# Kernel optimization log

Hardware: AMD Instinct MI355X
Metric: run time of the kernel (lower is better)

## Reference

```python
import jax, jax.numpy as jnp
import numpy as np

B, S, E, P, H, F = 4, 4096, 256, 32, 8, 1024
DH = E // H
LN_EPS = 1e-5


def setup_inputs() -> dict:
    key = jax.random.key(0)
    ks = jax.random.split(key, 12)
    dt = jnp.float32
    return {
        "src": jax.random.normal(ks[0], (B, S, E), dt),
        "pos_embed": jax.random.normal(ks[1], (B, P, S), dt),
        # learnable positional transform (pos_linear: P -> P)
        "Wpos": jax.random.normal(ks[2], (P, P), dt) * (1.0 / np.sqrt(P)),
        "bpos": jnp.zeros((P,), dt),
        # RBF kernel hyperparameters (ScaleKernel(RBFKernel)) -- positive scalars
        "lengthscale": jnp.full((), 2.0, dt),
        "outputscale": jnp.full((), 1.0, dt),
        # value / output projections of multihead attention
        "Wv": jax.random.normal(ks[3], (E, E), dt) * (1.0 / np.sqrt(E)),
        "bv": jnp.zeros((E,), dt),
        "Wo": jax.random.normal(ks[4], (E, E), dt) * (1.0 / np.sqrt(E)),
        "bo": jnp.zeros((E,), dt),
        # feed-forward
        "W1": jax.random.normal(ks[5], (F, E), dt) * (1.0 / np.sqrt(E)),
        "b1": jnp.zeros((F,), dt),
        "W2": jax.random.normal(ks[6], (E, F), dt) * (1.0 / np.sqrt(F)),
        "b2": jnp.zeros((E,), dt),
        # layer norms
        "ln1_g": jnp.ones((E,), dt), "ln1_b": jnp.zeros((E,), dt),
        "ln2_g": jnp.ones((E,), dt), "ln2_b": jnp.zeros((E,), dt),
    }


def _layer_norm(x, g, b):
    mu = jnp.mean(x, -1, keepdims=True)
    var = jnp.mean(jnp.square(x - mu), -1, keepdims=True)
    return (x - mu) * jax.lax.rsqrt(var + LN_EPS) * g + b


def _rbf_scores(x, lengthscale, outputscale):
    # x: [B, S, P] -> scaled RBF kernel matrix [B, S, S]
    xs = x / lengthscale
    sq = jnp.sum(xs * xs, axis=-1)  # [B, S]
    d2 = sq[:, :, None] + sq[:, None, :] - 2.0 * jnp.einsum('bsp,btp->bst', xs, xs)
    d2 = jnp.maximum(d2, 0.0)
    return outputscale * jnp.exp(-0.5 * d2)


def reference(src, pos_embed, Wpos, bpos, lengthscale, outputscale,
              Wv, bv, Wo, bo, W1, b1, W2, b2, ln1_g, ln1_b, ln2_g, ln2_b):
    b, s, e = src.shape
    # learnable positional transform: [B,P,S] -> [B,S,P] -> linear -> back
    pe = jnp.einsum('bps,op->bos', pos_embed, Wpos) + bpos[None, :, None]  # [B,P,S]
    # GP-kernel attention scores over sequence positions
    scores = _rbf_scores(pe.transpose(0, 2, 1), lengthscale, outputscale)  # [B,S,S]
    attn = jax.nn.softmax(scores, axis=-1)
    # value projection, per-head weighted sum (scores shared across heads)
    v = (src @ Wv.T + bv).reshape(b, s, H, DH)
    ctx = jnp.einsum('bqk,bkhd->bqhd', attn, v).reshape(b, s, e)
    attn_out = ctx @ Wo.T + bo
    x = _layer_norm(src + attn_out, ln1_g, ln1_b)
    ff = jax.nn.relu(x @ W1.T + b1) @ W2.T + b2
    return _layer_norm(x + ff, ln2_g, ln2_b)
```

## Files before the change

kernel.cpp:

```cpp
#include <hip/hip_runtime.h>
#include <stdint.h>

#define BN 4
#define SN 4096
#define EN 256
#define PN 32
#define FN 1024
#define BS (BN*SN)
#define PAUG 64

typedef uint16_t bf16_t;
typedef short v4s  __attribute__((ext_vector_type(4)));
typedef short v8s  __attribute__((ext_vector_type(8)));
typedef __bf16 bf16x8 __attribute__((ext_vector_type(8)));
typedef float v4f   __attribute__((ext_vector_type(4)));
typedef float v16f  __attribute__((ext_vector_type(16)));

#define MFMA16(a,b,c) __builtin_amdgcn_mfma_f32_16x16x32_bf16(a,b,c,0,0,0)
#define MFMA32(a,b,c) __builtin_amdgcn_mfma_f32_32x32x16_bf16(a,b,c,0,0,0)

__device__ __forceinline__ float b2f(bf16_t x){
    uint32_t u = ((uint32_t)x) << 16; float f; __builtin_memcpy(&f, &u, 4); return f;
}
__device__ __forceinline__ bf16_t f2b(float f){
    uint32_t u; __builtin_memcpy(&u, &f, 4);
    u += 0x7FFFu + ((u >> 16) & 1u);
    return (bf16_t)(u >> 16);
}
__device__ __forceinline__ bf16x8 ldb8(const bf16_t* p){
    v8s r = *(const v8s*)p; return __builtin_bit_cast(bf16x8, r);
}
__device__ __forceinline__ bf16x8 ldb8u(const bf16_t* p){
    v4s lo = *(const v4s*)p;
    v4s hi = *(const v4s*)(p + 4);
    v8s r = __builtin_shufflevector(lo, hi, 0,1,2,3,4,5,6,7);
    return __builtin_bit_cast(bf16x8, r);
}
__device__ __forceinline__ float ldsc(const float* p){ return *p; }
__device__ __forceinline__ float ldsc(const bf16_t* p){ return b2f(*p); }
__device__ __forceinline__ void stsc(float* p, float v){ *p = v; }
__device__ __forceinline__ void stsc(bf16_t* p, float v){ *p = f2b(v); }

#if __has_builtin(__builtin_amdgcn_exp2f)
__device__ __forceinline__ float fexp2(float x){ return __builtin_amdgcn_exp2f(x); }
#else
__device__ __forceinline__ float fexp2(float x){ return exp2f(x); }
#endif

#if __has_builtin(__builtin_amdgcn_cvt_pk_bf16_f32)
typedef __bf16 bf16x2 __attribute__((ext_vector_type(2)));
__device__ __forceinline__ uint32_t pkbf16(float a, float b){
    bf16x2 r = __builtin_amdgcn_cvt_pk_bf16_f32(a, b);
    return __builtin_bit_cast(uint32_t, r);
}
#else
__device__ __forceinline__ uint32_t pkbf16(float a, float b){
    return (uint32_t)f2b(a) | ((uint32_t)f2b(b) << 16);
}
#endif

typedef const __attribute__((address_space(1))) uint32_t* glds_gp;
typedef __attribute__((address_space(3))) uint32_t* glds_lp;
__device__ __forceinline__ void glds16(const bf16_t* g, bf16_t* l){
    __builtin_amdgcn_global_load_lds((glds_gp)g, (glds_lp)l, 16, 0, 0);
}

__global__ __launch_bounds__(256) void prep_kernel(
    const float* __restrict__ src, bf16_t* __restrict__ srcb,
    const float* __restrict__ Wv, bf16_t* __restrict__ Wvb,
    const float* __restrict__ Wo, bf16_t* __restrict__ Wob,
    const float* __restrict__ W1, bf16_t* __restrict__ W1b,
    const float* __restrict__ W2, bf16_t* __restrict__ W2b,
    const float* __restrict__ pos, const float* __restrict__ Wp,
    const float* __restrict__ bp,  const float* __restrict__ lsp,
    bf16_t* __restrict__ xk, bf16_t* __restrict__ xq)
{
    __shared__ float Wsh[PN*PN];
    __shared__ float bsh[PN];
    int bid = blockIdx.x;
    int tid = threadIdx.x;

    if (bid < 4736){
        const float* sp; bf16_t* dp; int off;
        if (bid < 4096){ sp = src; dp = srcb; off = (bid*256 + tid)*4; }
        else {
            int i = ((bid - 4096)*256 + tid)*4;
            if      (i <  65536){ sp=Wv; dp=Wvb; off=i; }
            else if (i < 131072){ sp=Wo; dp=Wob; off=i- 65536; }
            else if (i < 393216){ sp=W1; dp=W1b; off=i-131072; }
            else                { sp=W2; dp=W2b; off=i-393216; }
        }
        float4 f = *(const float4*)(sp + off);
        v4s o;
        o.x = (short)f2b(f.x); o.y = (short)f2b(f.y);
        o.z = (short)f2b(f.z); o.w = (short)f2b(f.w);
        *(v4s*)(dp + off) = o;
        return;
    }

    int pb = bid - 4736;
    int b  = pb >> 4;
    int s  = (pb & 15)*256 + tid;

    for (int i = tid; i < PN*PN; i += 256) Wsh[i] = Wp[i];
    if (tid < PN) bsh[tid] = bp[tid];
    __syncthreads();

    float inv_ls = 1.0f / lsp[0];
    const float c1f = 1.4426950408889634f;

    float col[PN];
    #pragma unroll
    for (int p = 0; p < PN; p++) col[p] = pos[((size_t)b*PN + p)*SN + s];

    uint16_t xb[PN], qb[PN];
    float sq = 0.f;
    #pragma unroll 4
    for (int o = 0; o < PN; o++){
        float pe = bsh[o];
        #pragma unroll
        for (int p = 0; p < PN; p++) pe += col[p] * Wsh[o*PN + p];
        float pv = pe * inv_ls;
        uint16_t h = f2b(pv);
        xb[o] = h;
        qb[o] = f2b(c1f * pv);
        float xr = b2f(h);
        sq += xr * xr;
    }

    size_t base = ((size_t)b*SN + s) * PAUG;
    v8s pk[8];
    #pragma unroll
    for (int c = 0; c < 4; c++)
        #pragma unroll
        for (int j = 0; j < 8; j++) ((short*)&pk[c])[j] = (short)xb[c*8 + j];
    #pragma unroll
    for (int c = 4; c < 8; c++)
        #pragma unroll
        for (int j = 0; j < 8; j++) ((short*)&pk[c])[j] = 0;
    ((short*)&pk[4])[0] = (short)f2b(-0.5f * sq);
    ((short*)&pk[4])[1] = (short)0x3F80;
    #pragma unroll
    for (int c = 0; c < 8; c++) *(v8s*)(xk + base + c*8) = pk[c];

    #pragma unroll
    for (int c = 0; c < 4; c++)
        #pragma unroll
        for (int j = 0; j < 8; j++) ((short*)&pk[c])[j] = (short)qb[c*8 + j];
    ((short*)&pk[4])[0] = (short)f2b(c1f);
    ((short*)&pk[4])[1] = (short)f2b(-0.5f * sq * c1f);
    #pragma unroll
    for (int c = 0; c < 8; c++) *(v8s*)(xq + base + c*8) = pk[c];
}

template<int EPI, typename OutT>
__global__ __launch_bounds__(256) void gemm_t(
    const bf16_t* __restrict__ A, const bf16_t* __restrict__ W,
    const float* __restrict__ bias, OutT* __restrict__ out,
    bf16_t* __restrict__ vt, int N, int K)
{
    __shared__ __align__(16) bf16_t At[2][4096];
    __shared__ __align__(16) bf16_t Wt[2][4096];
    int tid = threadIdx.x;
    int lane = tid & 63, wv = tid >> 6, col = lane & 15, quad = lane >> 4;
    int m0 = blockIdx.x * 64, n0 = blockIdx.y * 64;
    int nck = K >> 6;

    int srow = tid >> 3;
    int spc  = (tid & 7) ^ (srow & 7);
    const bf16_t* asrc = A + (size_t)(m0 + srow)*K + spc*8;
    const bf16_t* wsrc = W + (size_t)(n0 + srow)*K + spc*8;

    v4f acc[4];
    #pragma unroll
    for (int t = 0; t < 4; t++) acc[t] = (v4f){0.f,0.f,0.f,0.f};

    glds16(asrc, &At[0][tid*8]);
    glds16(asrc + (size_t)32*K, &At[0][2048 + tid*8]);
    glds16(wsrc, &Wt[0][tid*8]);
    glds16(wsrc + (size_t)32*K, &Wt[0][2048 + tid*8]);
    __syncthreads();

    for (int c = 0; c < nck; c++){
        int cb = c & 1;
        if (c + 1 < nck){
            glds16(asrc + (c+1)*64, &At[cb^1][tid*8]);
            glds16(asrc + (size_t)32*K + (c+1)*64, &At[cb^1][2048 + tid*8]);
            glds16(wsrc + (c+1)*64, &Wt[cb^1][tid*8]);
            glds16(wsrc + (size_t)32*K + (c+1)*64, &Wt[cb^1][2048 + tid*8]);
        }
        #pragma unroll
        for (int kc = 0; kc < 2; kc++){
            int pc = ((kc*4 + quad) ^ (col & 7)) * 8;
            bf16x8 a = ldb8(&At[cb][(wv*16 + col)*64 + pc]);
            #pragma unroll
            for (int t = 0; t < 4; t++){
                bf16x8 b = ldb8(&Wt[cb][(t*16 + col)*64 + pc]);
                acc[t] = MFMA16(a, b, acc[t]);
            }
        }
        __syncthreads();
    }

    float bfv[4];
    #pragma unroll
    for (int t = 0; t < 4; t++) bfv[t] = bias[n0 + t*16 + col];

    if constexpr (EPI == 3){
        __shared__ uint16_t Tsh[64*74];
        #pragma unroll
        for (int r = 0; r < 4; r++)
            #pragma unroll
            for (int t = 0; t < 4; t++)
                Tsh[(wv*16 + quad*4 + r)*74 + t*16 + col] = f2b(acc[t][r] + bfv[t]);
        __syncthreads();
        int e = tid >> 2, sc = tid & 3;
        int b = m0 >> 12;
        int sbat = m0 & (SN-1);
        int eb   = (n0 + e) >> 5;
        int l31e = (n0 + e) & 31;
        int k16  = (sbat >> 4) + sc;
        v8s p0, p1;
        #pragma unroll
        for (int i = 0; i < 8; i++) ((short*)&p0)[i] = (short)Tsh[(sc*16 + i)*74 + e];
        #pragma unroll
        for (int i = 0; i < 8; i++) ((short*)&p1)[i] = (short)Tsh[(sc*16 + 8 + i)*74 + e];
        bf16_t* dst = vt + ((((size_t)b*8 + eb)*256 + k16)*64 + l31e)*8;
        *(v8s*)dst = p0;
        *(v8s*)(dst + 256) = p1;
    } else {
        #pragma unroll
        for (int r = 0; r < 4; r++){
            int row = m0 + wv*16 + quad*4 + r;
            #pragma unroll
            for (int t = 0; t < 4; t++){
                float y = acc[t][r] + bfv[t];
                if constexpr (EPI == 1) y = fmaxf(y, 0.f);
                stsc(out + (size_t)row*N + n0 + t*16 + col, y);
            }
        }
    }
}

template<int EPI>
__global__ __launch_bounds__(256, 2) void gemm128(
    const bf16_t* __restrict__ A, const bf16_t* __restrict__ W,
    const float* __restrict__ bias, bf16_t* __restrict__ out,
    int N, int K)
{
    __shared__ __align__(16) bf16_t At[2][8192];
    __shared__ __align__(16) bf16_t Wt[2][8192];
    int tid = threadIdx.x;
    int lane = tid & 63, wv = tid >> 6, col = lane & 15, quad = lane >> 4;
    int m0 = blockIdx.x * 128, n0 = blockIdx.y * 128;
    int nck = K >> 6;

    int srow = tid >> 3;
    int spc  = (tid & 7) ^ (srow & 7);
    const bf16_t* asrc = A + (size_t)(m0 + srow)*K + spc*8;
    const bf16_t* wsrc = W + (size_t)(n0 + srow)*K + spc*8;

    v4f acc[2][8];
    #pragma unroll
    for (int mi = 0; mi < 2; mi++)
        #pragma unroll
        for (int t = 0; t < 8; t++) acc[mi][t] = (v4f){0.f,0.f,0.f,0.f};

    #pragma unroll
    for (int s = 0; s < 4; s++){
        glds16(asrc + (size_t)(s*32)*K, &At[0][s*2048 + tid*8]);
        glds16(wsrc + (size_t)(s*32)*K, &Wt[0][s*2048 + tid*8]);
    }
    __syncthreads();

    for (int c = 0; c < nck; c++){
        int cb = c & 1;
        if (c + 1 < nck){
            #pragma unroll
            for (int s = 0; s < 4; s++){
                glds16(asrc + (size_t)(s*32)*K + (c+1)*64, &At[cb^1][s*2048 + tid*8]);
                glds16(wsrc + (size_t)(s*32)*K + (c+1)*64, &Wt[cb^1][s*2048 + tid*8]);
            }
        }
        #pragma unroll
        for (int kc = 0; kc < 2; kc++){
            int pc = ((kc*4 + quad) ^ (col & 7)) * 8;
            bf16x8 a[2];
            #pragma unroll
            for (int mi = 0; mi < 2; mi++)
                a[mi] = ldb8(&At[cb][(wv*32 + mi*16 + col)*64 + pc]);
            #pragma unroll
            for (int t = 0; t < 8; t++){
                bf16x8 b = ldb8(&Wt[cb][(t*16 + col)*64 + pc]);
                #pragma unroll
                for (int mi = 0; mi < 2; mi++)
                    acc[mi][t] = MFMA16(a[mi], b, acc[mi][t]);
            }
        }
        __syncthreads();
    }

    float bfv[8];
    #pragma unroll
    for (int t = 0; t < 8; t++) bfv[t] = bias[n0 + t*16 + col];

    #pragma unroll
    for (int mi = 0; mi < 2; mi++){
        #pragma unroll
        for (int r = 0; r < 4; r++){
            int row = m0 + wv*32 + mi*16 + quad*4 + r;
            #pragma unroll
            for (int t = 0; t < 8; t++){
                float y = acc[mi][t][r] + bfv[t];
                if constexpr (EPI == 1) y = fmaxf(y, 0.f);
                out[(size_t)row*N + n0 + t*16 + col] = f2b(y);
            }
        }
    }
}

template<typename OutT>
__global__ __launch_bounds__(512, 4) void gemm_ln(
    const bf16_t* __restrict__ A, const bf16_t* __restrict__ W,
    const float* __restrict__ bias, const bf16_t* __restrict__ res,
    const float* __restrict__ gamma, const float* __restrict__ beta,
    OutT* __restrict__ out, int K)
{
    __shared__ __align__(16) bf16_t At[2][32*64];
    __shared__ __align__(16) bf16_t Wt[2][256*64];
    __shared__ float lnb[4][32][2];

    int tid = threadIdx.x;
    int lane = tid & 63, wv = tid >> 6, col = lane & 15, quad = lane >> 4;
    int mw = wv >> 2;
    int nw = wv & 3;
    int m0 = blockIdx.x * 32;
    int nck = K >> 6;

    int arow = (tid & 255) >> 3;
    int apc  = (tid & 7) ^ (arow & 7);
    const bf16_t* asrc = A + (size_t)(m0 + arow)*K + apc*8;
    int wr0  = tid >> 3;
    const bf16_t* wsrc[4];
    #pragma unroll
    for (int s = 0; s < 4; s++){
        int wrow = s*64 + wr0;
        int wpc  = (tid & 7) ^ (wrow & 7);
        wsrc[s] = W + (size_t)wrow*K + wpc*8;
    }

    v4f acc[4];
    #pragma unroll
    for (int t = 0; t < 4; t++) acc[t] = (v4f){0.f,0.f,0.f,0.f};

    if (tid < 256) glds16(asrc, &At[0][tid*8]);
    #pragma unroll
    for (int s = 0; s < 4; s++) glds16(wsrc[s], &Wt[0][s*4096 + tid*8]);
    __syncthreads();

    for (int c = 0; c < nck; c++){
        int cb = c & 1;
        if (c + 1 < nck){
            if (tid < 256) glds16(asrc + (c+1)*64, &At[cb^1][tid*8]);
            #pragma unroll
            for (int s = 0; s < 4; s++)
                glds16(wsrc[s] + (c+1)*64, &Wt[cb^1][s*4096 + tid*8]);
        }
        #pragma unroll
        for (int kc = 0; kc < 2; kc++){
            int pc = ((kc*4 + quad) ^ (col & 7)) * 8;
            bf16x8 a = ldb8(&At[cb][(mw*16 + col)*64 + pc]);
            #pragma unroll
            for (int t = 0; t < 4; t++){
                bf16x8 b = ldb8(&Wt[cb][(nw*64 + t*16 + col)*64 + pc]);
                acc[t] = MFMA16(a, b, acc[t]);
            }
        }
        __syncthreads();
    }

    float bfv[4];
    #pragma unroll
    for (int t = 0; t < 4; t++) bfv[t] = bias[nw*64 + t*16 + col];

    float v[4][4];
    float s1[4], s2[4];
    #pragma unroll
    for (int r = 0; r < 4; r++){ s1[r] = 0.f; s2[r] = 0.f; }
    #pragma unroll
    for (int r = 0; r < 4; r++){
        int row = m0 + mw*16 + quad*4 + r;
        #pragma unroll
        for (int t = 0; t < 4; t++){
            float x = acc[t][r] + bfv[t]
                    + b2f(res[(size_t)row*EN + nw*64 + t*16 + col]);
            v[t][r] = x; s1[r] += x; s2[r] += x*x;
        }
    }
    #pragma unroll
    for (int r = 0; r < 4; r++){
        #pragma unroll
        for (int m = 1; m <= 8; m <<= 1){
            s1[r] += __shfl_xor(s1[r], m);
            s2[r] += __shfl_xor(s2[r], m);
        }
    }
    if (col == 0){
        #pragma unroll
        for (int r = 0; r < 4; r++){
            int rl = mw*16 + quad*4 + r;
            lnb[nw][rl][0] = s1[r];
            lnb[nw][rl][1] = s2[r];
        }
    }
    __syncthreads();
    #pragma unroll
    for (int r = 0; r < 4; r++){
        int rl  = mw*16 + quad*4 + r;
        int row = m0 + rl;
        float S1 = lnb[0][rl][0] + lnb[1][rl][0] + lnb[2][rl][0] + lnb[3][rl][0];
        float S2 = lnb[0][rl][1] + lnb[1][rl][1] + lnb[2][rl][1] + lnb[3][rl][1];
        float mu = S1 * (1.f/256.f);
        float rs = rsqrtf(S2 * (1.f/256.f) - mu*mu + 1e-5f);
        #pragma unroll
        for (int t = 0; t < 4; t++){
            int gi = nw*64 + t*16 + col;
            stsc(out + (size_t)row*EN + gi, (v[t][r]-mu)*rs*gamma[gi] + beta[gi]);
        }
    }
}

__global__ __launch_bounds__(512, 4) void attn_kernel(
    const bf16_t* __restrict__ xk, const bf16_t* __restrict__ xq,
    const bf16_t* __restrict__ vf, const float* __restrict__ osp,
    bf16_t* __restrict__ ctx)
{
    __shared__ __align__(16) bf16_t Wtb[2][64*132];
    __shared__ __align__(16) bf16_t Qs[64*64];
    __shared__ float densh[8][64];
    __shared__ float dent[64];

    int tid  = threadIdx.x;
    int lane = tid & 63;
    int wv   = tid >> 6;
    int col  = lane & 15;
    int quad = lane >> 4;
    int l31  = lane & 31;
    int half = lane >> 5;

    int bid = blockIdx.x;
    int b   = (bid & 7) >> 1;
    int qi  = ((bid >> 3) << 1) | (bid & 1);
    int q0  = qi * 64;

    float k2 = 1.4426950408889634f * osp[0];

    const bf16_t* xkb = xk + (size_t)b * SN * PAUG;
    const bf16_t* xqb = xq + (size_t)b * SN * PAUG;
    const bf16_t* vfb = vf + (((size_t)b*8 + wv)*256)*512 + lane*8;

    {
        int qrow = tid >> 3;
        int qpc  = (tid & 7) ^ (qrow & 7);
        glds16(xqb + (size_t)(q0 + qrow)*PAUG + qpc*8, &Qs[tid*8]);
    }

    v16f acc[2];
    #pragma unroll
    for (int qg = 0; qg < 2; qg++)
        #pragma unroll
        for (int i = 0; i < 16; i++) acc[qg][i] = 0.f;
    float den[4] = {0.f, 0.f, 0.f, 0.f};
    const v4f zero = (v4f){0.f,0.f,0.f,0.f};

    bf16x8 kf0, kf1;
    {
        const bf16_t* kr = xkb + (size_t)(wv*16 + col)*PAUG + quad*8;
        kf0 = ldb8(kr); kf1 = ldb8(kr + 32);
    }

    __syncthreads();

    for (int c = 0; c < 32; c++){
        int cb = c & 1;
        bf16x8 vr[8];
        #pragma unroll
        for (int sk = 0; sk < 8; sk++)
            vr[sk] = ldb8(vfb + (size_t)(c*8 + sk)*512);

        #pragma unroll
        for (int qg = 0; qg < 2; qg++){
            #pragma unroll
            for (int g2 = 0; g2 < 2; g2++){
                int qr = qg*32 + g2*16 + col;
                bf16x8 qa = ldb8(&Qs[qr*64 + ((quad    ) ^ (col & 7))*8]);
                bf16x8 qb = ldb8(&Qs[qr*64 + ((4 + quad) ^ (col & 7))*8]);
                v4f st = MFMA16(kf0, qa, zero);
                st = MFMA16(kf1, qb, st);
                #pragma unroll
                for (int rp = 0; rp < 2; rp++){
                    float w0 = fexp2(fmaf(k2, fexp2(st[rp*2+0]), -k2));
                    float w1 = fexp2(fmaf(k2, fexp2(st[rp*2+1]), -k2));
                    den[qg*2+g2] += w0 + w1;
                    *(uint32_t*)&Wtb[cb][qr*132 + wv*16 + quad*4 + rp*2]
                        = pkbf16(w0, w1);
                }
            }
        }

        if (c + 1 < 32){
            const bf16_t* kr = xkb + (size_t)((c+1)*128 + wv*16 + col)*PAUG + quad*8;
            kf0 = ldb8(kr); kf1 = ldb8(kr + 32);
        }

        asm volatile("s_waitcnt lgkmcnt(0)" ::: "memory");
        __builtin_amdgcn_s_barrier();
        __builtin_amdgcn_sched_barrier(0);

        #pragma unroll
        for (int qg = 0; qg < 2; qg++){
            #pragma unroll
            for (int sk4 = 0; sk4 < 2; sk4++){
                bf16x8 af[4];
                #pragma unroll
                for (int j = 0; j < 4; j++)
                    af[j] = ldb8u(&Wtb[cb][(qg*32 + l31)*132 + (sk4*4 + j)*16 + half*8]);
                #pragma unroll
                for (int j = 0; j < 4; j++)
                    acc[qg] = MFMA32(af[j], vr[sk4*4 + j], acc[qg]);
            }
        }
    }

    #pragma unroll
    for (int d = 0; d < 4; d++){
        den[d] += __shfl_xor(den[d], 16);
        den[d] += __shfl_xor(den[d], 32);
    }
    if (lane < 16){
        #pragma unroll
        for (int qg = 0; qg < 2; qg++)
            #pragma unroll
            for (int g2 = 0; g2 < 2; g2++)
                densh[wv][qg*32 + g2*16 + lane] = den[qg*2+g2];
    }
    __syncthreads();
    if (tid < 64){
        float s = 0.f;
        #pragma unroll
        for (int w = 0; w < 8; w++) s += densh[w][tid];
        dent[tid] = 1.f / s;
    }
    __syncthreads();

    size_t obase = ((size_t)b*SN + q0) * EN + wv*32;
    #pragma unroll
    for (int qg = 0; qg < 2; qg++){
        #pragma unroll
        for (int rg = 0; rg < 16; rg++){
            int row = (rg & 3) + 8*(rg >> 2) + 4*half;
            float inv = dent[qg*32 + row];
            ctx[obase + (size_t)(qg*32 + row)*EN + l31] = f2b(acc[qg][rg] * inv);
        }
    }
}

extern "C" void kernel_launch(void* const* d_in, const int* in_sizes, int n_in,
                              void* d_out, int out_size, void* d_ws, size_t ws_size,
                              hipStream_t stream)
{
    (void)in_sizes; (void)n_in; (void)out_size; (void)ws_size;
    const float* src  = (const float*)d_in[0];
    const float* pos  = (const float*)d_in[1];
    const float* Wpos = (const float*)d_in[2];
    const float* bpos = (const float*)d_in[3];
    const float* ls   = (const float*)d_in[4];
    const float* os   = (const float*)d_in[5];
    const float* Wv   = (const float*)d_in[6];
    const float* bv   = (const float*)d_in[7];
    const float* Wo   = (const float*)d_in[8];
    const float* bo   = (const float*)d_in[9];
    const float* W1   = (const float*)d_in[10];
    const float* b1   = (const float*)d_in[11];
    const float* W2   = (const float*)d_in[12];
    const float* b2   = (const float*)d_in[13];
    const float* g1   = (const float*)d_in[14];
    const float* be1  = (const float*)d_in[15];
    const float* g2   = (const float*)d_in[16];
    const float* be2  = (const float*)d_in[17];

    char* w = (char*)d_ws;
    bf16_t* xkb  = (bf16_t*)(w);
    bf16_t* xqb  = (bf16_t*)(w + ( 2u<<20));
    bf16_t* Wvb  = (bf16_t*)(w + ( 4u<<20));
    bf16_t* Wob  = (bf16_t*)(w + ( 4u<<20) + (1u<<18));
    bf16_t* W1b  = (bf16_t*)(w + ( 5u<<20));
    bf16_t* W2b  = (bf16_t*)(w + ( 6u<<20));
    bf16_t* srcb = (bf16_t*)(w + ( 8u<<20));
    bf16_t* vtg  = (bf16_t*)(w + (16u<<20));
    bf16_t* ctx  = (bf16_t*)(w + (24u<<20));
    bf16_t* xws  = (bf16_t*)(w + (24u<<20));
    bf16_t* hws  = (bf16_t*)(w + (32u<<20));

    prep_kernel<<<dim3(4800), 256, 0, stream>>>(
        src, srcb, Wv, Wvb, Wo, Wob, W1, W1b, W2, W2b,
        pos, Wpos, bpos, ls, xkb, xqb);

    gemm_t<3, bf16_t><<<dim3(BS/64, EN/64), 256, 0, stream>>>(
        srcb, Wvb, bv, (bf16_t*)nullptr, vtg, EN, EN);
    attn_kernel<<<dim3(256), 512, 0, stream>>>(xkb, xqb, vtg, os, ctx);
    gemm_ln<bf16_t><<<dim3(BS/32), 512, 0, stream>>>(
        ctx, Wob, bo, srcb, g1, be1, xws, EN);
    gemm128<1><<<dim3(BS/128, FN/128), 256, 0, stream>>>(
        xws, W1b, b1, hws, FN, EN);
    gemm_ln<float><<<dim3(BS/32), 512, 0, stream>>>(
        hws, W2b, b2, xws, g2, be2, (float*)d_out, FN);
}
```

Baseline: 232.5 us.

## Fuse output projection, residual and LayerNorm into attention kernel epilogue

The attention kernel now writes its normalized context tile into shared memory and runs the Wo projection with MFMA, then adds bias and residual and applies LayerNorm 1 before writing x. This removes the ctx round trip through global memory and one kernel launch. Wo is pre-swizzled into an MFMA-fragment layout in the prep kernel, and launch bounds drop from 4 to 2 blocks per CU. The extra 32KB of shared memory and added registers may reduce occupancy of the attention phase.

```diff
diff --git a/kernel.cpp b/kernel.cpp
--- a/kernel.cpp
+++ b/kernel.cpp
@@ -86,7 +86,17 @@
         else {
             int i = ((bid - 4096)*256 + tid)*4;
             if      (i <  65536){ sp=Wv; dp=Wvb; off=i; }
-            else if (i < 131072){ sp=Wo; dp=Wob; off=i- 65536; }
+            else if (i < 131072){
+                int idx = i - 65536;
+                float4 f = *(const float4*)(Wo + idx);
+                v4s o;
+                o.x = (short)f2b(f.x); o.y = (short)f2b(f.y);
+                o.z = (short)f2b(f.z); o.w = (short)f2b(f.w);
+                int n = idx >> 8, k = idx & 255;
+                int dst = (((n>>4)*8 + (k>>5))*64 + (((k>>3)&3)*16 + (n&15)))*8 + (k&7);
+                *(v4s*)(Wob + dst) = o;
+                return;
+            }
             else if (i < 393216){ sp=W1; dp=W1b; off=i-131072; }
             else                { sp=W2; dp=W2b; off=i-393216; }
         }
@@ -430,15 +440,19 @@
     }
 }
 
-__global__ __launch_bounds__(512, 4) void attn_kernel(
+__global__ __launch_bounds__(512, 2) void attn_kernel(
     const bf16_t* __restrict__ xk, const bf16_t* __restrict__ xq,
     const bf16_t* __restrict__ vf, const float* __restrict__ osp,
-    bf16_t* __restrict__ ctx)
+    const bf16_t* __restrict__ wof, const float* __restrict__ bo,
+    const bf16_t* __restrict__ res, const float* __restrict__ gamma,
+    const float* __restrict__ beta, bf16_t* __restrict__ out)
 {
     __shared__ __align__(16) bf16_t Wtb[2][64*132];
     __shared__ __align__(16) bf16_t Qs[64*64];
+    __shared__ __align__(16) bf16_t Osh[64*256];
     __shared__ float densh[8][64];
     __shared__ float dent[64];
+    __shared__ float lnw[8][64][2];
 
     int tid  = threadIdx.x;
     int lane = tid & 63;
@@ -553,14 +567,74 @@
     }
     __syncthreads();
 
-    size_t obase = ((size_t)b*SN + q0) * EN + wv*32;
     #pragma unroll
     for (int qg = 0; qg < 2; qg++){
         #pragma unroll
         for (int rg = 0; rg < 16; rg++){
-            int row = (rg & 3) + 8*(rg >> 2) + 4*half;
-            float inv = dent[qg*32 + row];
-            ctx[obase + (size_t)(qg*32 + row)*EN + l31] = f2b(acc[qg][rg] * inv);
+            int qrow = qg*32 + (rg & 3) + 8*(rg >> 2) + 4*half;
+            int e = wv*32 + l31;
+            int g = e >> 3;
+            Osh[qrow*256 + ((g ^ (qrow & 7))*8) + (e & 7)] = f2b(acc[qg][rg] * dent[qrow]);
+        }
+    }
+    __syncthreads();
+
+    v4f y[4][2];
+    #pragma unroll
+    for (int qg = 0; qg < 4; qg++)
+        #pragma unroll
+        for (int t = 0; t < 2; t++) y[qg][t] = (v4f){0.f,0.f,0.f,0.f};
+
+    #pragma unroll
+    for (int kc = 0; kc < 8; kc++){
+        bf16x8 b0 = ldb8(wof + (size_t)(((wv*2+0)*8 + kc)*64 + lane)*8);
+        bf16x8 b1 = ldb8(wof + (size_t)(((wv*2+1)*8 + kc)*64 + lane)*8);
+        #pragma unroll
+        for (int qg = 0; qg < 4; qg++){
+            bf16x8 a = ldb8(&Osh[(qg*16 + col)*256 + (((kc*4 + quad) ^ (col & 7))*8)]);
+            y[qg][0] = MFMA16(a, b0, y[qg][0]);
+            y[qg][1] = MFMA16(a, b1, y[qg][1]);
+        }
+    }
+
+    size_t growb = (size_t)b*SN + q0;
+    float bo0 = bo[wv*32 + col], bo1 = bo[wv*32 + 16 + col];
+    #pragma unroll
+    for (int qg = 0; qg < 4; qg++){
+        #pragma unroll
+        for (int r = 0; r < 4; r++){
+            int row = qg*16 + quad*4 + r;
+            float x0 = y[qg][0][r] + bo0 + b2f(res[(growb + row)*EN + wv*32 + col]);
+            float x1 = y[qg][1][r] + bo1 + b2f(res[(growb + row)*EN + wv*32 + 16 + col]);
+            y[qg][0][r] = x0; y[qg][1][r] = x1;
+            float s1 = x0 + x1, s2 = x0*x0 + x1*x1;
+            #pragma unroll
+            for (int m = 1; m <= 8; m <<= 1){
+                s1 += __shfl_xor(s1, m);
+                s2 += __shfl_xor(s2, m);
+            }
+            if (col == 0){
+                lnw[wv][row][0] = s1;
+                lnw[wv][row][1] = s2;
+            }
+        }
+    }
+    __syncthreads();
+
+    float g0 = gamma[wv*32 + col],      g1v = gamma[wv*32 + 16 + col];
+    float e0 = beta[wv*32 + col],       e1v = beta[wv*32 + 16 + col];
+    #pragma unroll
+    for (int qg = 0; qg < 4; qg++){
+        #pragma unroll
+        for (int r = 0; r < 4; r++){
+            int row = qg*16 + quad*4 + r;
+            float S1 = 0.f, S2 = 0.f;
+            #pragma unroll
+            for (int w = 0; w < 8; w++){ S1 += lnw[w][row][0]; S2 += lnw[w][row][1]; }
+            float mu = S1 * (1.f/256.f);
+            float rs = rsqrtf(S2 * (1.f/256.f) - mu*mu + 1e-5f);
+            out[(growb + row)*EN + wv*32 + col]      = f2b((y[qg][0][r]-mu)*rs*g0 + e0);
+            out[(growb + row)*EN + wv*32 + 16 + col] = f2b((y[qg][1][r]-mu)*rs*g1v + e1v);
         }
     }
 }
@@ -598,7 +672,6 @@
     bf16_t* W2b  = (bf16_t*)(w + ( 6u<<20));
     bf16_t* srcb = (bf16_t*)(w + ( 8u<<20));
     bf16_t* vtg  = (bf16_t*)(w + (16u<<20));
-    bf16_t* ctx  = (bf16_t*)(w + (24u<<20));
     bf16_t* xws  = (bf16_t*)(w + (24u<<20));
     bf16_t* hws  = (bf16_t*)(w + (32u<<20));
 
@@ -608,9 +681,8 @@
 
     gemm_t<3, bf16_t><<<dim3(BS/64, EN/64), 256, 0, stream>>>(
         srcb, Wvb, bv, (bf16_t*)nullptr, vtg, EN, EN);
-    attn_kernel<<<dim3(256), 512, 0, stream>>>(xkb, xqb, vtg, os, ctx);
-    gemm_ln<bf16_t><<<dim3(BS/32), 512, 0, stream>>>(
-        ctx, Wob, bo, srcb, g1, be1, xws, EN);
+    attn_kernel<<<dim3(256), 512, 0, stream>>>(
+        xkb, xqb, vtg, os, Wob, bo, srcb, g1, be1, xws);
     gemm128<1><<<dim3(BS/128, FN/128), 256, 0, stream>>>(
         xws, W1b, b1, hws, FN, EN);
     gemm_ln<float><<<dim3(BS/32), 512, 0, stream>>>(
```

After: 231.9 us. About the same (-0.3%).
